# Optimization experiments

Hardware: AMD Instinct MI355X
Metric: run time of the kernel (lower is better)

## Reference

```python
import jax, jax.numpy as jnp
import numpy as np

B, T, N, F_FEAT = 2, 1024, 263, 2
D = 263                # d_model
C = N * F_FEAT         # 526 = d_model * n_features
WINDOW = 25
K_T = int(T * 0.1)     # temporal masked steps
K_F = int(T * 0.1)     # masked frequency bins (<= T//2+1)


def positional_encoding(t, d):
    pos = jnp.arange(t, dtype=jnp.float32)[:, None]
    div = jnp.exp(jnp.arange(0, d, 2, dtype=jnp.float32) * (-np.log(10000.0) / d))
    pe = jnp.zeros((t, d), dtype=jnp.float32)
    pe = pe.at[:, 0::2].set(jnp.sin(pos * div))
    n_odd = pe[:, 1::2].shape[1]
    pe = pe.at[:, 1::2].set(jnp.cos(pos * div[:n_odd]))
    return pe


def setup_inputs() -> dict:
    key = jax.random.key(0)
    ks = jax.random.split(key, 10)
    s = 0.02
    return {
        "x": jax.random.normal(ks[0], (B, T, N, F_FEAT), dtype=jnp.float32),
        "W_emb": jax.random.normal(ks[1], (D, C), dtype=jnp.float32) * s,
        "b_emb": jnp.zeros((D,), jnp.float32),
        "t_token": jax.random.normal(ks[2], (D,), dtype=jnp.float32) * s,
        "W1t": jax.random.normal(ks[3], (D, D), dtype=jnp.float32) * s,
        "b1t": jnp.zeros((D,), jnp.float32),
        "W2t": jax.random.normal(ks[4], (D, D), dtype=jnp.float32) * s,
        "b2t": jnp.zeros((D,), jnp.float32),
        "f_token_r": jax.random.normal(ks[5], (D,), dtype=jnp.float32) * s,
        "f_token_i": jax.random.normal(ks[6], (D,), dtype=jnp.float32) * s,
        "w1f": jax.random.normal(ks[7], (D,), dtype=jnp.float32) * s,
        "b1f": jnp.zeros((D,), jnp.float32),
        "w2f": jax.random.normal(ks[8], (D,), dtype=jnp.float32) * s,
        "b2f": jnp.zeros((1,), jnp.float32),
    }


def _forward(x, W_emb, b_emb, t_token, W1t, b1t, W2t, b2t,
             f_token_r, f_token_i, w1f, b1f, w2f, b2f):
    pe = positional_encoding(T, D)
    # DataEmbedding (dropout inactive / eval) + positional embedding
    ex = x.reshape(B, T, C) @ W_emb.T + b_emb + pe            # [B,T,D]
    bidx = jnp.arange(B)[:, None]

    # ---- temporal masking: causal sliding mean/var (== conv1d ones kernel) ----
    counts = jnp.minimum(jnp.arange(T, dtype=jnp.float32) + 1.0, float(WINDOW))[None, :, None]

    def causal_mean(v):
        cs = jnp.cumsum(v, axis=1)
        shifted = jnp.concatenate([jnp.zeros((B, WINDOW, D), v.dtype), cs[:, :-WINDOW]], axis=1)
        return (cs - shifted) / counts

    m1 = causal_mean(ex)
    var = causal_mean(ex * ex) - m1 * m1
    score = var.sum(-1) / (m1.sum(-1) + 1e-6)                 # [B,T]
    _, idx_t = jax.lax.top_k(score, K_T)                      # [B,K_T]
    masked = ex.at[bidx, idx_t].set(t_token)
    mask_t = jnp.zeros((B, T), bool).at[bidx, idx_t].set(True)
    h = jax.nn.gelu(masked @ W1t.T + b1t, approximate=False)
    proj = jax.nn.sigmoid(h @ W2t.T + b2t)
    masked = jnp.where(mask_t[..., None], masked, proj)
    out_t = (masked @ W_emb).reshape(B, T, N, F_FEAT)         # weight.T @ x^T, transposed

    # ---- frequency masking ----
    cx = jnp.fft.rfft(ex, axis=1)                             # [B, T//2+1, D]
    mag = jnp.abs(cx)
    _, idx_f = jax.lax.top_k(mag.mean(axis=2), K_F)           # [B,K_F]
    token_c = (f_token_r + 1j * f_token_i).astype(cx.dtype)
    cxm = cx.at[bidx, idx_f].set(token_c)
    xt = jnp.fft.irfft(cxm, n=T, axis=1)                      # [B,T,D]
    fm = jnp.zeros((B, T // 2 + 1), jnp.float32).at[bidx, idx_f].set(1.0)
    mask_f = jnp.fft.irfft(fm, n=T, axis=1) != 0              # [B,T] (same for all channels)
    v = xt @ W_emb                                            # [B,T,C]
    # per-scalar MLP: Linear(1,D)+GELU+Linear(D,1)+Sigmoid
    hf = jax.nn.gelu(v[..., None] * w1f + b1f, approximate=False)   # [B,T,C,D]
    projf = jax.nn.sigmoid(jnp.einsum('btcd,d->btc', hf, w2f) + b2f)
    out_f = jnp.where(mask_f[:, :, None], v, projf).reshape(B, T, N, F_FEAT)

    return out_t, idx_t, out_f, idx_f


def reference(x, W_emb, b_emb, t_token, W1t, b1t, W2t, b2t,
              f_token_r, f_token_i, w1f, b1f, w2f, b2f):
    return _forward(x, W_emb, b_emb, t_token, W1t, b1t, W2t, b2t,
                    f_token_r, f_token_i, w1f, b1f, w2f, b2f)
```

## Files before the change

kernel.cpp:

```cpp
#include <hip/hip_runtime.h>

#define TDIM 1024
#define DD   263
#define CC   526
#define NFREQ 513
#define PACK 1026
#define KTOP 102

static const size_t WS_EX     = 0;
static const size_t WS_W1BF   = 538624;
static const size_t WS_W2BF   = 584704;
static const size_t WS_WEMT   = 630784;
static const size_t WS_MASKB  = 1615872;
static const size_t WS_XTBF   = 1910784;
static const size_t WS_HBF    = 2693120;
static const size_t WS_CXP    = 3770368;
static const size_t WS_EXTHL  = 4310044;
static const size_t WS_ITSEL  = 5360668;
static const size_t WS_DELTA  = 5901340;
static const size_t WS_TABC   = 6411292;
static const size_t WS_TABS   = 6412316;
static const size_t WS_SCORE  = 6413340;
static const size_t WS_MAGM   = 6417436;
static const size_t WS_MASKT  = 6419488;
static const size_t WS_IDXT   = 6421536;
static const size_t WS_IDXF   = 6421740;
static const size_t WS_MASKF  = 6421944;
static const size_t WS_XHL    = 6422972;
static const size_t WS_THL    = 8094140;
static const size_t WS_WHL    = 9765308;
static const size_t WS_TOTAL  = 10740380;

static const size_t OFF_OUTT = 0;
static const size_t OFF_IDXT = 1077248;
static const size_t OFF_OUTF = 1077452;
static const size_t OFF_IDXF = 2154700;

typedef __bf16 bf16x8_t __attribute__((ext_vector_type(8)));
typedef float  f32x4_t  __attribute__((ext_vector_type(4)));

__device__ __forceinline__ unsigned short f2bf(float f) {
    unsigned int u = __float_as_uint(f);
    unsigned int r = (u + 0x7fffu + ((u >> 16) & 1u)) >> 16;
    return (unsigned short)r;
}
__device__ __forceinline__ float bf2f(unsigned short h) {
    return __uint_as_float(((unsigned int)h) << 16);
}

__device__ __forceinline__ float pe_val(int t, int d) {
    const float sc = (float)(-9.210340371976184 / 263.0);
    int j = d >> 1;
    float div = expf((float)(2 * j) * sc);
    float a = (float)t * div;
    return (d & 1) ? cosf(a) : sinf(a);
}

#define WG_FENCE()   asm volatile("" ::: "memory")
#define WG_BARRIER() { WG_FENCE(); __builtin_amdgcn_s_barrier(); WG_FENCE(); }

template<int EPI, int KU>
__device__ __forceinline__ void gemm_body(int hw, int nwg,
                                          const unsigned short* __restrict__ A,
                                          const unsigned short* __restrict__ Bt,
                                          const float* __restrict__ bias,
                                          void* __restrict__ Cv,
                                          void* __restrict__ aux,
                                          int M, int N, int SA, int NC, int gy)
{
    __shared__ unsigned short As[64][32 * KU + 8];
    __shared__ unsigned short Bs[64][32 * KU + 8];
    const int q = nwg >> 3, r = nwg & 7, xcd = hw & 7;
    const int logical = (xcd < r ? xcd * (q + 1) : r * (q + 1) + (xcd - r) * q) + (hw >> 3);
    const int row0 = (logical / gy) * 64, col0 = (logical % gy) * 64;
    if (EPI == 7) Bt += (size_t)(row0 >> 10) * 320 * SA;

    const int tid  = threadIdx.x;
    const int wid = tid >> 6, lane = tid & 63;
    const int wr = wid >> 1, wc = wid & 1;
    const int srow = tid >> 2, skoff = (tid & 3) * 8;
    const int fl = lane & 15, fh = lane >> 4;
    f32x4_t acc[2][2];
#pragma unroll
    for (int i = 0; i < 2; i++)
#pragma unroll
        for (int j = 0; j < 2; j++) acc[i][j] = (f32x4_t){0.f, 0.f, 0.f, 0.f};

    const int nk = SA / (32 * KU);
    const unsigned short* pa = A  + (size_t)(row0 + srow) * SA + skoff;
    const unsigned short* pb = Bt + (size_t)(col0 + srow) * SA + skoff;

    bf16x8_t qa[4][KU], qb[4][KU];
#pragma unroll
    for (int j = 0; j < 4; ++j) {
        if (j < nk) {
#pragma unroll
            for (int u = 0; u < KU; ++u) {
                qa[j][u] = *(const bf16x8_t*)(pa + (size_t)j * (32 * KU) + u * 32);
                qb[j][u] = *(const bf16x8_t*)(pb + (size_t)j * (32 * KU) + u * 32);
            }
        }
    }

    for (int itb = 0; itb < nk; itb += 4) {
#pragma unroll
        for (int j = 0; j < 4; ++j) {
            const int it = itb + j;
            if (it < nk) {
                if (it > 0) WG_BARRIER();
#pragma unroll
                for (int u = 0; u < KU; ++u) {
                    *(bf16x8_t*)(&As[srow][u * 32 + skoff]) = qa[j][u];
                    *(bf16x8_t*)(&Bs[srow][u * 32 + skoff]) = qb[j][u];
                }
                asm volatile("s_waitcnt lgkmcnt(0)" ::: "memory");
                WG_BARRIER();
#pragma unroll
                for (int u = 0; u < KU; ++u) {
                    bf16x8_t fa0 = *(const bf16x8_t*)(&As[wr * 32 + fl][u * 32 + fh * 8]);
                    bf16x8_t fa1 = *(const bf16x8_t*)(&As[wr * 32 + 16 + fl][u * 32 + fh * 8]);
                    bf16x8_t fb0 = *(const bf16x8_t*)(&Bs[wc * 32 + fl][u * 32 + fh * 8]);
                    bf16x8_t fb1 = *(const bf16x8_t*)(&Bs[wc * 32 + 16 + fl][u * 32 + fh * 8]);
                    acc[0][0] = __builtin_amdgcn_mfma_f32_16x16x32_bf16(fa0, fb0, acc[0][0], 0, 0, 0);
                    acc[0][1] = __builtin_amdgcn_mfma_f32_16x16x32_bf16(fa0, fb1, acc[0][1], 0, 0, 0);
                    acc[1][0] = __builtin_amdgcn_mfma_f32_16x16x32_bf16(fa1, fb0, acc[1][0], 0, 0, 0);
                    acc[1][1] = __builtin_amdgcn_mfma_f32_16x16x32_bf16(fa1, fb1, acc[1][1], 0, 0, 0);
                }
                if (it + 4 < nk) {
#pragma unroll
                    for (int u = 0; u < KU; ++u) {
                        qa[j][u] = *(const bf16x8_t*)(pa + (size_t)(it + 4) * (32 * KU) + u * 32);
                        qb[j][u] = *(const bf16x8_t*)(pb + (size_t)(it + 4) * (32 * KU) + u * 32);
                    }
                }
            }
        }
    }

#pragma unroll
    for (int fi = 0; fi < 2; fi++)
#pragma unroll
        for (int fj = 0; fj < 2; fj++)
#pragma unroll
            for (int rr = 0; rr < 4; rr++) {
                int m = row0 + wr * 32 + fi * 16 + fh * 4 + rr;
                int n = col0 + wc * 32 + fj * 16 + fl;
                if (m >= M) continue;
                float v = acc[fi][fj][rr];
                if (EPI == 0) {
                    if (n < N) ((float*)Cv)[(size_t)m * NC + n] = v;
                } else if (EPI == 1) {
                    if (n < NC) {
                        float o = 0.0f;
                        if (n < N) { o = v + bias[n]; o = 0.5f * o * (1.0f + erff(o * 0.70710678118654752f)); }
                        ((unsigned short*)Cv)[(size_t)m * NC + n] = f2bf(o);
                    }
                } else if (EPI == 4) {
                    if (n < N) {
                        float o = v + bias[n] + pe_val(m & (TDIM - 1), n);
                        ((float*)Cv)[(size_t)m * NC + n] = o;
                        unsigned short hi = f2bf(o);
                        unsigned short lo = f2bf(o - bf2f(hi));
                        size_t b2 = ((size_t)(m >> 10) * 320 + n) * 3072 + (m & 1023);
                        unsigned short* xh = (unsigned short*)aux;
                        xh[b2] = hi; xh[b2 + 1024] = lo; xh[b2 + 2048] = hi;
                    }
                } else if (EPI == 5) {
                    int b = n / 320, col = n - b * 320;
                    if (col < DD) ((float*)Cv)[((size_t)b * PACK + m) * DD + col] = v;
                } else if (EPI == 7) {
                    if (n < 288) {
                        unsigned short o = 0;
                        if (n < DD) o = f2bf(bias[(size_t)m * DD + n] + v);
                        ((unsigned short*)Cv)[(size_t)m * 288 + n] = o;
                    }
                } else if (EPI == 8) {
                    const int* mt = (const int*)aux;
                    if (n < 288 && !mt[m]) {
                        unsigned short o = 0;
                        if (n < DD) {
                            float s = v + bias[n];
                            o = f2bf(1.0f / (1.0f + expf(-s)));
                        }
                        ((unsigned short*)Cv)[(size_t)m * 288 + n] = o;
                    }
                } else {
                    if (n < CC) {
                        size_t off = (m < 2048) ? (size_t)m * CC + n
                                                : (size_t)OFF_OUTF + (size_t)(m - 2048) * CC + n;
                        ((float*)Cv)[off] = v;
                    }
                }
            }
}

template<int EPI, int KU>
__global__ __launch_bounds__(256) void gemm_k(const unsigned short* __restrict__ A,
                                              const unsigned short* __restrict__ Bt,
                                              const float* __restrict__ bias,
                                              void* __restrict__ Cv, void* __restrict__ aux,
                                              int M, int N, int SA, int NC, int gy)
{
    gemm_body<EPI, KU>(blockIdx.x, gridDim.x, A, Bt, bias, Cv, aux, M, N, SA, NC, gy);
}

__device__ __forceinline__ void score_wave(int ib, const float* __restrict__ ex,
                                           double* __restrict__ score) {
    const int t = ib & (TDIM - 1);
    const int lane = threadIdx.x & 63;
    double ms = 0.0, vs = 0.0;
    if (t >= 24) {
        const float* base = ex + (size_t)(ib - 24) * DD;
        for (int d = lane; d < DD; d += 64) {
            float s1 = 0.0f, s2 = 0.0f;
#pragma unroll
            for (int r = 0; r < 25; r++) {
                float v = base[(size_t)r * DD + d];
                s1 += v;
                s2 += v * v;
            }
            float m1 = s1 * (1.0f / 25.0f);
            float var = s2 * (1.0f / 25.0f) - m1 * m1;
            ms += (double)m1;
            vs += (double)var;
        }
    } else {
        const int nt = t + 1;
        const float cnt = (float)nt;
        const float* base = ex + (size_t)(ib - t) * DD;
        for (int d = lane; d < DD; d += 64) {
            float s1 = 0.0f, s2 = 0.0f;
            for (int r = 0; r < nt; r++) {
                float v = base[(size_t)r * DD + d];
                s1 += v;
                s2 += v * v;
            }
            float m1 = s1 / cnt;
            float var = s2 / cnt - m1 * m1;
            ms += (double)m1;
            vs += (double)var;
        }
    }
#pragma unroll
    for (int off = 32; off; off >>= 1) { ms += __shfl_xor(ms, off); vs += __shfl_xor(vs, off); }
    if (lane == 0) score[ib] = vs / (ms + (double)1e-6f);
}

__device__ __forceinline__ void mag_wave(int ib, const float* __restrict__ cxp,
                                         double* __restrict__ magm) {
    int b = ib / NFREQ, k = ib % NFREQ;
    int lane = threadIdx.x & 63;
    const float* re = cxp + ((size_t)b * PACK + k) * DD;
    const float* im = cxp + ((size_t)b * PACK + NFREQ + k) * DD;
    double acc = 0.0;
    for (int d = lane; d < DD; d += 64) {
        float r = re[d], i = im[d];
        acc += (double)sqrtf(r * r + i * i);
    }
#pragma unroll
    for (int off = 32; off; off >>= 1) acc += __shfl_xor(acc, off);
    if (lane == 0) magm[ib] = acc / (double)DD;
}

__device__ __forceinline__ void topk_body(int b, const double* __restrict__ score,
                                          int n, int kcount,
                                          float* __restrict__ out_f, int* __restrict__ out_i,
                                          int* __restrict__ mask) {
    __shared__ double sv[1024];
    __shared__ int    si[1024];
    const int tid = threadIdx.x;
    const double* s = score + (size_t)b * n;
    for (int i = tid; i < 1024; i += 512) {
        sv[i] = (i < n) ? s[i] : -1.0e300;
        si[i] = i;
    }
    __syncthreads();
    for (int k = 2; k <= 1024; k <<= 1) {
        for (int j = k >> 1; j > 0; j >>= 1) {
            int t = ((tid & ~(j - 1)) << 1) | (tid & (j - 1));
            int l = t | j;
            double v0 = sv[t], v1 = sv[l];
            int i0 = si[t], i1 = si[l];
            bool g = (v0 > v1) || (v0 == v1 && i0 < i1);
            bool wrong = ((t & k) == 0) ? !g : g;
            if (wrong) {
                sv[t] = v1; sv[l] = v0;
                si[t] = i1; si[l] = i0;
            }
            __syncthreads();
        }
    }
    for (int t = tid; t < kcount; t += 512) {
        int bi = si[t];
        out_f[(size_t)b * kcount + t] = (float)bi;
        out_i[b * kcount + t] = bi;
        mask[b * n + bi] = 1;
    }
}

__device__ __forceinline__ void build_masked_body(int bt, const float* __restrict__ ex,
                                                  const float* __restrict__ ttok,
                                                  const int* __restrict__ maskt,
                                                  unsigned short* __restrict__ mb) {
    int d = threadIdx.x;
    if (d >= 288) return;
    float v = 0.0f;
    if (d < DD) v = maskt[bt] ? ttok[d] : ex[(size_t)bt * DD + d];
    mb[(size_t)bt * 288 + d] = f2bf(v);
}

__device__ __forceinline__ void sel_delta_body(int blk,
                                               const float* __restrict__ tabc, const float* __restrict__ tabs,
                                               const int* __restrict__ idxf, const float* __restrict__ cxp,
                                               const float* __restrict__ ftr, const float* __restrict__ fti,
                                               unsigned short* __restrict__ itsel,
                                               unsigned short* __restrict__ delta) {
    if (blk < 2048) {
        int b = blk >> 10, t = blk & 1023;
        unsigned short* dst = itsel + (size_t)blk * 224;
        for (int j = threadIdx.x; j < 224; j += 256) {
            float v = 0.0f;
            if (j < KTOP) {
                int k = idxf[b * KTOP + j];
                float w = (k == 0 || k == 512) ? 1.0f : 2.0f;
                v = (w * (1.0f / 1024.0f)) * tabc[(k * t) & 1023];
            } else if (j >= 112 && j < 112 + KTOP) {
                int k = idxf[b * KTOP + j - 112];
                v = (k == 0 || k == 512) ? 0.0f : (-2.0f / 1024.0f) * tabs[(k * t) & 1023];
            }
            dst[j] = f2bf(v);
        }
    } else {
        int idx = blk - 2048;
        int b = idx / 320, d = idx - (idx / 320) * 320;
        unsigned short* dst = delta + (size_t)idx * 224;
        for (int j = threadIdx.x; j < 224; j += 256) {
            float v = 0.0f;
            if (d < DD) {
                if (j < KTOP) {
                    int k = idxf[b * KTOP + j];
                    v = ftr[d] - cxp[((size_t)b * PACK + k) * DD + d];
                } else if (j >= 112 && j < 112 + KTOP) {
                    int k = idxf[b * KTOP + j - 112];
                    v = fti[d] - cxp[((size_t)b * PACK + NFREQ + k) * DD + d];
                }
            }
            dst[j] = f2bf(v);
        }
    }
}

__global__ __launch_bounds__(256) void fused_dft_score_k(const unsigned short* __restrict__ thl,
                                                         const unsigned short* __restrict__ exthl,
                                                         float* __restrict__ cxp,
                                                         const float* __restrict__ ex,
                                                         double* __restrict__ score)
{
    if (blockIdx.x < 170) {
        gemm_body<5, 4>(blockIdx.x, 170, thl, exthl, nullptr, cxp, nullptr, PACK, 640, 3072, 0, 10);
    } else {
        int ib = (int)(blockIdx.x - 170) * 4 + (threadIdx.x >> 6);
        score_wave(ib, ex, score);
    }
}

__global__ __launch_bounds__(512) void fused_topkt_mag_k(const double* __restrict__ score,
                                                         float* __restrict__ outf, int* __restrict__ idxt,
                                                         int* __restrict__ maskt,
                                                         const float* __restrict__ cxp,
                                                         double* __restrict__ magm)
{
    if (blockIdx.x < 2) {
        topk_body(blockIdx.x, score, TDIM, KTOP, outf, idxt, maskt);
    } else {
        int ib = (int)(blockIdx.x - 2) * 8 + (threadIdx.x >> 6);
        if (ib < 2 * NFREQ) mag_wave(ib, cxp, magm);
    }
}

__global__ __launch_bounds__(512) void fused_topkf_bm_k(const double* __restrict__ magm,
                                                        float* __restrict__ outf, int* __restrict__ idxf,
                                                        int* __restrict__ maskf,
                                                        const float* __restrict__ ex,
                                                        const float* __restrict__ ttok,
                                                        const int* __restrict__ maskt,
                                                        unsigned short* __restrict__ mb)
{
    if (blockIdx.x < 2) {
        topk_body(blockIdx.x, magm, NFREQ, KTOP, outf, idxf, maskf);
    } else {
        build_masked_body(blockIdx.x - 2, ex, ttok, maskt, mb);
    }
}

__global__ __launch_bounds__(256) void fused_h_seldelta_k(const unsigned short* __restrict__ maskb,
                                                          const unsigned short* __restrict__ w1b,
                                                          const float* __restrict__ b1t,
                                                          unsigned short* __restrict__ hb,
                                                          const float* __restrict__ tabc,
                                                          const float* __restrict__ tabs,
                                                          const int* __restrict__ idxf,
                                                          const float* __restrict__ cxp,
                                                          const float* __restrict__ ftr,
                                                          const float* __restrict__ fti,
                                                          unsigned short* __restrict__ itsel,
                                                          unsigned short* __restrict__ delta)
{
    if (blockIdx.x < 160) {
        gemm_body<1, 3>(blockIdx.x, 160, maskb, w1b, b1t, hb, nullptr, 2048, DD, 288, 288, 5);
    } else {
        sel_delta_body(blockIdx.x - 160, tabc, tabs, idxf, cxp, ftr, fti, itsel, delta);
    }
}

__global__ __launch_bounds__(256) void fused_sig_corr_k(const unsigned short* __restrict__ hb,
                                                        const unsigned short* __restrict__ w2b,
                                                        const float* __restrict__ b2t,
                                                        unsigned short* __restrict__ maskb,
                                                        const int* __restrict__ maskt,
                                                        const unsigned short* __restrict__ itsel,
                                                        const unsigned short* __restrict__ delta,
                                                        const float* __restrict__ ex,
                                                        unsigned short* __restrict__ xtb)
{
    if (blockIdx.x < 160) {
        gemm_body<8, 3>(blockIdx.x, 160, hb, w2b, b2t, maskb, (void*)maskt, 2048, DD, 288, 288, 5);
    } else {
        gemm_body<7, 1>(blockIdx.x - 160, 160, itsel, delta, ex, xtb, nullptr, 2048, 320, 224, 288, 5);
    }
}

__global__ void init0_k(int* maskt, int* maskf, float* tabc, float* tabs) {
    int i = blockIdx.x * 256 + threadIdx.x;
    if (i < 2 * TDIM) maskt[i] = 0;
    if (i < PACK) maskf[i] = 0;
    if (i < 1024) {
        double ang = (double)i * (3.14159265358979323846 * 2.0 / 1024.0);
        tabc[i] = (float)cos(ang);
        tabs[i] = (float)sin(ang);
    }
}

__global__ void convall_k(const float* __restrict__ tabc, const float* __restrict__ tabs,
                          const float* __restrict__ W1t, const float* __restrict__ W2t,
                          const float* __restrict__ W_emb, const float* __restrict__ x,
                          unsigned short* __restrict__ thl,
                          unsigned short* __restrict__ w1b, unsigned short* __restrict__ w2b,
                          unsigned short* __restrict__ wemT,
                          unsigned short* __restrict__ xhl, unsigned short* __restrict__ whl)
{
    int blk = blockIdx.x;
    if (blk < 1088) {
        int row = blk;
        unsigned short* dst = thl + (size_t)row * 3072;
        for (int c = threadIdx.x; c < 3072; c += 256) {
            int seg = c >> 10, t = c & 1023;
            float v = 0.0f;
            if (row < PACK) v = (row < NFREQ) ? tabc[(row * t) & 1023] : -tabs[((row - NFREQ) * t) & 1023];
            unsigned short hi = f2bf(v);
            dst[c] = (seg < 2) ? hi : f2bf(v - bf2f(hi));
        }
    } else if (blk < 2304) {
        int r = blk - 1088;
        if (r < 640) {
            int rr = r & 319;
            const float* src = (r < 320) ? W1t : W2t;
            unsigned short* dst = (r < 320) ? w1b : w2b;
            for (int c = threadIdx.x; c < 288; c += 256) {
                float v = (rr < DD && c < DD) ? src[(size_t)rr * DD + c] : 0.0f;
                dst[(size_t)rr * 288 + c] = f2bf(v);
            }
        } else {
            int rr = r - 640;
            for (int c = threadIdx.x; c < 288; c += 256) {
                float v = (rr < CC && c < DD) ? W_emb[(size_t)c * CC + rr] : 0.0f;
                wemT[(size_t)rr * 288 + c] = f2bf(v);
            }
        }
    } else if (blk < 4352) {
        int r = blk - 2304;
        const float* src = x + (size_t)r * CC;
        unsigned short* dst = xhl + (size_t)r * 1632;
        for (int c = threadIdx.x; c < 1632; c += 256) {
            int seg = c / 544, cc = c - seg * 544;
            float v = (cc < CC) ? src[cc] : 0.0f;
            unsigned short hi = f2bf(v);
            dst[c] = (seg < 2) ? hi : f2bf(v - bf2f(hi));
        }
    } else {
        int n = blk - 4352;
        unsigned short* dst = whl + (size_t)n * 1632;
        for (int c = threadIdx.x; c < 1632; c += 256) {
            int seg = c / 544, cc = c - seg * 544;
            float v = (n < DD && cc < CC) ? W_emb[(size_t)n * CC + cc] : 0.0f;
            unsigned short hi = f2bf(v);
            dst[c] = (seg == 1) ? f2bf(v - bf2f(hi)) : hi;
        }
    }
}

extern "C" void kernel_launch(void* const* d_in, const int* in_sizes, int n_in,
                              void* d_out, int out_size, void* d_ws, size_t ws_size,
                              hipStream_t stream) {
    (void)in_sizes; (void)n_in; (void)out_size; (void)ws_size;
    const float* x      = (const float*)d_in[0];
    const float* W_emb  = (const float*)d_in[1];
    const float* b_emb  = (const float*)d_in[2];
    const float* ttok   = (const float*)d_in[3];
    const float* W1t    = (const float*)d_in[4];
    const float* b1t    = (const float*)d_in[5];
    const float* W2t    = (const float*)d_in[6];
    const float* b2t    = (const float*)d_in[7];
    const float* ftr    = (const float*)d_in[8];
    const float* fti    = (const float*)d_in[9];
    float* out = (float*)d_out;
    float* ws  = (float*)d_ws;

    float* ex     = ws + WS_EX;
    float* cxp    = ws + WS_CXP;
    float* tabc   = ws + WS_TABC;
    float* tabs   = ws + WS_TABS;
    double* score = (double*)(ws + WS_SCORE);
    double* magm  = (double*)(ws + WS_MAGM);
    int* maskt    = (int*)(ws + WS_MASKT);
    int* idxt     = (int*)(ws + WS_IDXT);
    int* idxf     = (int*)(ws + WS_IDXF);
    int* maskf    = (int*)(ws + WS_MASKF);
    unsigned short* w1b   = (unsigned short*)(ws + WS_W1BF);
    unsigned short* w2b   = (unsigned short*)(ws + WS_W2BF);
    unsigned short* wemT  = (unsigned short*)(ws + WS_WEMT);
    unsigned short* maskb = (unsigned short*)(ws + WS_MASKB);
    unsigned short* hb    = (unsigned short*)(ws + WS_HBF);
    unsigned short* xtb   = (unsigned short*)(ws + WS_XTBF);
    unsigned short* itsel = (unsigned short*)(ws + WS_ITSEL);
    unsigned short* delta = (unsigned short*)(ws + WS_DELTA);
    unsigned short* xhl   = (unsigned short*)(ws + WS_XHL);
    unsigned short* thl   = (unsigned short*)(ws + WS_THL);
    unsigned short* whl   = (unsigned short*)(ws + WS_WHL);
    unsigned short* exthl = (unsigned short*)(ws + WS_EXTHL);

    init0_k<<<8, 256, 0, stream>>>(maskt, maskf, tabc, tabs);
    convall_k<<<4672, 256, 0, stream>>>(tabc, tabs, W1t, W2t, W_emb, x,
                                        thl, w1b, w2b, wemT, xhl, whl);

    gemm_k<4, 3><<<160, 256, 0, stream>>>(xhl, whl, b_emb, ex, exthl, 2048, DD, 1632, DD, 5);

    fused_dft_score_k<<<682, 256, 0, stream>>>(thl, exthl, cxp, ex, score);

    fused_topkt_mag_k<<<131, 512, 0, stream>>>(score, out + OFF_IDXT, idxt, maskt, cxp, magm);

    fused_topkf_bm_k<<<2050, 512, 0, stream>>>(magm, out + OFF_IDXF, idxf, maskf,
                                               ex, ttok, maskt, maskb);

    fused_h_seldelta_k<<<2848, 256, 0, stream>>>(maskb, w1b, b1t, hb,
                                                 tabc, tabs, idxf, cxp, ftr, fti, itsel, delta);

    fused_sig_corr_k<<<320, 256, 0, stream>>>(hb, w2b, b2t, maskb, maskt,
                                              itsel, delta, ex, xtb);

    gemm_k<9, 3><<<576, 256, 0, stream>>>(maskb, wemT, nullptr, out, nullptr, 4096, CC, 288, CC, 9);
}
```

Before: 125.3 us.

## Merge init and conversion kernels, overlap DFT table build with embedding GEMM

Folds the init kernel into the conversion kernel, and moves construction of the DFT twiddle table (thl) out of that kernel into extra blocks running alongside the embedding GEMM. This removes one launch and lets the table build overlap with the GEMM. The bitonic top-k sort now uses a wave-local LDS wait instead of a full workgroup barrier when the compare stride stays inside one wave. That wave-only sync depends on wavefront-size assumptions about which threads touch which elements.

```diff
diff --git a/kernel.cpp b/kernel.cpp
--- a/kernel.cpp
+++ b/kernel.cpp
@@ -58,6 +58,7 @@
 
 #define WG_FENCE()   asm volatile("" ::: "memory")
 #define WG_BARRIER() { WG_FENCE(); __builtin_amdgcn_s_barrier(); WG_FENCE(); }
+#define WAVE_LDS_SYNC() { asm volatile("s_waitcnt lgkmcnt(0)" ::: "memory"); __builtin_amdgcn_sched_barrier(0); }
 
 template<int EPI, int KU>
 __device__ __forceinline__ void gemm_body(int hw, int nwg,
@@ -287,9 +288,12 @@
                 sv[t] = v1; sv[l] = v0;
                 si[t] = i1; si[l] = i0;
             }
-            __syncthreads();
-        }
-    }
+            int next_j = (j > 1) ? (j >> 1) : k;
+            if (j >= 128 || next_j >= 128) __syncthreads();
+            else WAVE_LDS_SYNC();
+        }
+    }
+    __syncthreads();
     for (int t = tid; t < kcount; t += 512) {
         int bi = si[t];
         out_f[(size_t)b * kcount + t] = (float)bi;
@@ -350,6 +354,95 @@
     }
 }
 
+__device__ __forceinline__ void thl_row_body(int row, const float* __restrict__ tabc,
+                                             const float* __restrict__ tabs,
+                                             unsigned short* __restrict__ thl) {
+    unsigned short* dst = thl + (size_t)row * 3072;
+    for (int c = threadIdx.x; c < 3072; c += 256) {
+        int seg = c >> 10, t = c & 1023;
+        float v = 0.0f;
+        if (row < PACK) v = (row < NFREQ) ? tabc[(row * t) & 1023] : -tabs[((row - NFREQ) * t) & 1023];
+        unsigned short hi = f2bf(v);
+        dst[c] = (seg < 2) ? hi : f2bf(v - bf2f(hi));
+    }
+}
+
+__global__ __launch_bounds__(256) void initconv_k(int* maskt, int* maskf, float* tabc, float* tabs,
+                                                  const float* __restrict__ W1t,
+                                                  const float* __restrict__ W2t,
+                                                  const float* __restrict__ W_emb,
+                                                  const float* __restrict__ x,
+                                                  unsigned short* __restrict__ w1b,
+                                                  unsigned short* __restrict__ w2b,
+                                                  unsigned short* __restrict__ wemT,
+                                                  unsigned short* __restrict__ xhl,
+                                                  unsigned short* __restrict__ whl)
+{
+    int blk = blockIdx.x;
+    if (blk < 8) {
+        int i = blk * 256 + threadIdx.x;
+        if (i < 2 * TDIM) maskt[i] = 0;
+        if (i < PACK) maskf[i] = 0;
+        if (i < 1024) {
+            double ang = (double)i * (3.14159265358979323846 * 2.0 / 1024.0);
+            tabc[i] = (float)cos(ang);
+            tabs[i] = (float)sin(ang);
+        }
+    } else if (blk < 1224) {
+        int r = blk - 8;
+        if (r < 640) {
+            int rr = r & 319;
+            const float* src = (r < 320) ? W1t : W2t;
+            unsigned short* dst = (r < 320) ? w1b : w2b;
+            for (int c = threadIdx.x; c < 288; c += 256) {
+                float v = (rr < DD && c < DD) ? src[(size_t)rr * DD + c] : 0.0f;
+                dst[(size_t)rr * 288 + c] = f2bf(v);
+            }
+        } else {
+            int rr = r - 640;
+            for (int c = threadIdx.x; c < 288; c += 256) {
+                float v = (rr < CC && c < DD) ? W_emb[(size_t)c * CC + rr] : 0.0f;
+                wemT[(size_t)rr * 288 + c] = f2bf(v);
+            }
+        }
+    } else if (blk < 3272) {
+        int r = blk - 1224;
+        const float* src = x + (size_t)r * CC;
+        unsigned short* dst = xhl + (size_t)r * 1632;
+        for (int c = threadIdx.x; c < 1632; c += 256) {
+            int seg = c / 544, cc = c - seg * 544;
+            float v = (cc < CC) ? src[cc] : 0.0f;
+            unsigned short hi = f2bf(v);
+            dst[c] = (seg < 2) ? hi : f2bf(v - bf2f(hi));
+        }
+    } else {
+        int n = blk - 3272;
+        unsigned short* dst = whl + (size_t)n * 1632;
+        for (int c = threadIdx.x; c < 1632; c += 256) {
+            int seg = c / 544, cc = c - seg * 544;
+            float v = (n < DD && cc < CC) ? W_emb[(size_t)n * CC + cc] : 0.0f;
+            unsigned short hi = f2bf(v);
+            dst[c] = (seg == 1) ? f2bf(v - bf2f(hi)) : hi;
+        }
+    }
+}
+
+__global__ __launch_bounds__(256) void fused_ex_thl_k(const unsigned short* __restrict__ xhl,
+                                                      const unsigned short* __restrict__ whl,
+                                                      const float* __restrict__ b_emb,
+                                                      float* __restrict__ ex,
+                                                      unsigned short* __restrict__ exthl,
+                                                      const float* __restrict__ tabc,
+                                                      const float* __restrict__ tabs,
+                                                      unsigned short* __restrict__ thl)
+{
+    if (blockIdx.x < 160) {
+        gemm_body<4, 3>(blockIdx.x, 160, xhl, whl, b_emb, ex, exthl, 2048, DD, 1632, DD, 5);
+    } else {
+        thl_row_body(blockIdx.x - 160, tabc, tabs, thl);
+    }
+}
+
 __global__ __launch_bounds__(256) void fused_dft_score_k(const unsigned short* __restrict__ thl,
                                                          const unsigned short* __restrict__ exthl,
                                                          float* __restrict__ cxp,
@@ -427,75 +520,6 @@
         gemm_body<8, 3>(blockIdx.x, 160, hb, w2b, b2t, maskb, (void*)maskt, 2048, DD, 288, 288, 5);
     } else {
         gemm_body<7, 1>(blockIdx.x - 160, 160, itsel, delta, ex, xtb, nullptr, 2048, 320, 224, 288, 5);
-    }
-}
-
-__global__ void init0_k(int* maskt, int* maskf, float* tabc, float* tabs) {
-    int i = blockIdx.x * 256 + threadIdx.x;
-    if (i < 2 * TDIM) maskt[i] = 0;
-    if (i < PACK) maskf[i] = 0;
-    if (i < 1024) {
-        double ang = (double)i * (3.14159265358979323846 * 2.0 / 1024.0);
-        tabc[i] = (float)cos(ang);
-        tabs[i] = (float)sin(ang);
-    }
-}
-
-__global__ void convall_k(const float* __restrict__ tabc, const float* __restrict__ tabs,
-                          const float* __restrict__ W1t, const float* __restrict__ W2t,
-                          const float* __restrict__ W_emb, const float* __restrict__ x,
-                          unsigned short* __restrict__ thl,
-                          unsigned short* __restrict__ w1b, unsigned short* __restrict__ w2b,
-                          unsigned short* __restrict__ wemT,
-                          unsigned short* __restrict__ xhl, unsigned short* __restrict__ whl)
-{
-    int blk = blockIdx.x;
-    if (blk < 1088) {
-        int row = blk;
-        unsigned short* dst = thl + (size_t)row * 3072;
-        for (int c = threadIdx.x; c < 3072; c += 256) {
-            int seg = c >> 10, t = c & 1023;
-            float v = 0.0f;
-            if (row < PACK) v = (row < NFREQ) ? tabc[(row * t) & 1023] : -tabs[((row - NFREQ) * t) & 1023];
-            unsigned short hi = f2bf(v);
-            dst[c] = (seg < 2) ? hi : f2bf(v - bf2f(hi));
-        }
-    } else if (blk < 2304) {
-        int r = blk - 1088;
-        if (r < 640) {
-            int rr = r & 319;
-            const float* src = (r < 320) ? W1t : W2t;
-            unsigned short* dst = (r < 320) ? w1b : w2b;
-            for (int c = threadIdx.x; c < 288; c += 256) {
-                float v = (rr < DD && c < DD) ? src[(size_t)rr * DD + c] : 0.0f;
-                dst[(size_t)rr * 288 + c] = f2bf(v);
-            }
-        } else {
-            int rr = r - 640;
-            for (int c = threadIdx.x; c < 288; c += 256) {
-                float v = (rr < CC && c < DD) ? W_emb[(size_t)c * CC + rr] : 0.0f;
-                wemT[(size_t)rr * 288 + c] = f2bf(v);
-            }
-        }
-    } else if (blk < 4352) {
-        int r = blk - 2304;
-        const float* src = x + (size_t)r * CC;
-        unsigned short* dst = xhl + (size_t)r * 1632;
-        for (int c = threadIdx.x; c < 1632; c += 256) {
-            int seg = c / 544, cc = c - seg * 544;
-            float v = (cc < CC) ? src[cc] : 0.0f;
-            unsigned short hi = f2bf(v);
-            dst[c] = (seg < 2) ? hi : f2bf(v - bf2f(hi));
-        }
-    } else {
-        int n = blk - 4352;
-        unsigned short* dst = whl + (size_t)n * 1632;
-        for (int c = threadIdx.x; c < 1632; c += 256) {
-            int seg = c / 544, cc = c - seg * 544;
-            float v = (n < DD && cc < CC) ? W_emb[(size_t)n * CC + cc] : 0.0f;
-            unsigned short hi = f2bf(v);
-            dst[c] = (seg == 1) ? f2bf(v - bf2f(hi)) : hi;
-        }
     }
 }
 
@@ -539,11 +563,10 @@
     unsigned short* whl   = (unsigned short*)(ws + WS_WHL);
     unsigned short* exthl = (unsigned short*)(ws + WS_EXTHL);
 
-    init0_k<<<8, 256, 0, stream>>>(maskt, maskf, tabc, tabs);
-    convall_k<<<4672, 256, 0, stream>>>(tabc, tabs, W1t, W2t, W_emb, x,
-                                        thl, w1b, w2b, wemT, xhl, whl);
-
-    gemm_k<4, 3><<<160, 256, 0, stream>>>(xhl, whl, b_emb, ex, exthl, 2048, DD, 1632, DD, 5);
+    initconv_k<<<3592, 256, 0, stream>>>(maskt, maskf, tabc, tabs,
+                                         W1t, W2t, W_emb, x, w1b, w2b, wemT, xhl, whl);
+
+    fused_ex_thl_k<<<1248, 256, 0, stream>>>(xhl, whl, b_emb, ex, exthl, tabc, tabs, thl);
 
     fused_dft_score_k<<<682, 256, 0, stream>>>(thl, exthl, cxp, ex, score);
 
```

Result: faster. 114.4 us (median of 3 runs) (-8.7%).
